# Optimization experiments

Measured on AMD Instinct MI355X. Metric: run time of the kernel, lower is better.

Reference implementation:

```python
import jax, jax.numpy as jnp
import numpy as np

B, T, H = 2, 2048, 1024
NH = 16
D = H // NH  # head_dim = 64
SCALE = D ** -0.5


def setup_inputs() -> dict:
    key = jax.random.key(0)
    ks = jax.random.split(key, 10)
    s_in = 1.0 / np.sqrt(H)   # torch Linear init scale for fan_in=H
    s_d = 1.0 / np.sqrt(D)
    return {
        "x":  jax.random.normal(ks[0], (B, T, H), jnp.float32),
        # stacked per-head Q/K projections: [NH, H, D] weights, [NH, D] biases
        "Wq": jax.random.uniform(ks[1], (NH, H, D), jnp.float32, -s_in, s_in),
        "bq": jax.random.uniform(ks[2], (NH, D), jnp.float32, -s_in, s_in),
        "Wk": jax.random.uniform(ks[3], (NH, H, D), jnp.float32, -s_in, s_in),
        "bk": jax.random.uniform(ks[4], (NH, D), jnp.float32, -s_in, s_in),
        # shared V projection H->D
        "Wv": jax.random.uniform(ks[5], (H, D), jnp.float32, -s_in, s_in),
        "bv": jax.random.uniform(ks[6], (D,), jnp.float32, -s_in, s_in),
        # out projection D->H
        "Wo": jax.random.uniform(ks[7], (D, H), jnp.float32, -s_d, s_d),
        "bo": jax.random.uniform(ks[8], (H,), jnp.float32, -s_d, s_d),
    }


def reference(x, Wq, bq, Wk, bk, Wv, bv, Wo, bo):
    # shared value projection: [B,T,D]
    v = jnp.einsum('bth,hd->btd', x, Wv) + bv
    # batched per-head Q/K projections: [NH,B,T,D]
    q = jnp.einsum('bth,nhd->nbtd', x, Wq) + bq[:, None, None, :]
    k = jnp.einsum('bth,nhd->nbtd', x, Wk) + bk[:, None, None, :]
    # scaled causal attention scores: [NH,B,T,T]
    scores = jnp.einsum('nbtd,nbsd->nbts', q, k) * SCALE
    causal = jnp.triu(jnp.ones((T, T), bool), k=1)  # True above diagonal
    scores = jnp.where(causal, -jnp.inf, scores)
    weights = jax.nn.softmax(scores, axis=-1)  # dropout is identity in eval
    # shared V attended per head, then mean over heads: [B,T,D]
    mean_head = jnp.einsum('nbts,bsd->btd', weights, v) / NH
    out = jnp.einsum('btd,dh->bth', mean_head, Wo) + bo
    mean_weights = jnp.mean(weights, axis=0)  # [B,T,T]
    return out, mean_weights
```

## Files before the change

### kernel.cpp

```cpp
#include <hip/hip_runtime.h>
#include <hip/hip_bf16.h>

#define B_ 2
#define T_ 2048
#define H_ 1024
#define NH_ 16
#define D_ 64
#define BT_ (B_*T_)
#define SCALE_ 0.125f

typedef _Float16 f16x8 __attribute__((ext_vector_type(8)));
typedef float f32x4 __attribute__((ext_vector_type(4)));

#define MFMA(a,b,c) __builtin_amdgcn_mfma_f32_16x16x32_f16((a),(b),(c),0,0,0)

typedef const __attribute__((address_space(1))) void GV;
typedef __attribute__((address_space(3))) void LV;

__device__ __forceinline__ size_t toff(int r, int c, int C) {
    return (size_t)((r >> 4) * (C >> 5) + (c >> 5)) * 512 + (size_t)(((c & 31) >> 3) * 128 + (r & 15) * 8 + (c & 7));
}
__device__ __forceinline__ f16x8 frag_ld(const _Float16* base, int rt, int kc, int Cc, int l15, int quad) {
    return *(const f16x8*)(base + (size_t)(rt * Cc + kc) * 512 + quad * 128 + l15 * 8);
}

__global__ __launch_bounds__(256) void k_cast_x(const float* __restrict__ x, _Float16* __restrict__ xb) {
    int idx = blockIdx.x * 256 + threadIdx.x;
    int t = idx >> 7, h0 = (idx & 127) * 8;
    const float* p = x + ((size_t)t << 10) + h0;
    float4 f0 = *(const float4*)p;
    float4 f1 = *(const float4*)(p + 4);
    f16x8 o;
    o[0]=(_Float16)f0.x; o[1]=(_Float16)f0.y; o[2]=(_Float16)f0.z; o[3]=(_Float16)f0.w;
    o[4]=(_Float16)f1.x; o[5]=(_Float16)f1.y; o[6]=(_Float16)f1.z; o[7]=(_Float16)f1.w;
    *(f16x8*)(xb + toff(t, h0, 1024)) = o;
}

__global__ __launch_bounds__(256) void k_cast_wqk(const float* __restrict__ Wq, const float* __restrict__ Wk,
                                                  _Float16* __restrict__ wqk) {
    int idx = blockIdx.x * 256 + threadIdx.x;
    int head = idx >> 13;
    int rem = idx & 8191;
    int h = rem >> 3;
    int d0 = (rem & 7) * 8;
    const float* pq = Wq + ((size_t)((head << 10) + h)) * 64 + d0;
    const float* pk = Wk + ((size_t)((head << 10) + h)) * 64 + d0;
    float4 q0 = *(const float4*)pq, q1 = *(const float4*)(pq + 4);
    float4 k0 = *(const float4*)pk, k1 = *(const float4*)(pk + 4);
    float qv[8] = {q0.x,q0.y,q0.z,q0.w,q1.x,q1.y,q1.z,q1.w};
    float kv[8] = {k0.x,k0.y,k0.z,k0.w,k1.x,k1.y,k1.z,k1.w};
#pragma unroll
    for (int e = 0; e < 8; e++) {
        int c = head * 64 + d0 + e;
        wqk[toff(c, h, 1024)]        = (_Float16)qv[e];
        wqk[toff(c + 1024, h, 1024)] = (_Float16)kv[e];
    }
}

__global__ __launch_bounds__(256) void k_cast_wvo(const float* __restrict__ Wv, const float* __restrict__ Wo,
                                                  _Float16* __restrict__ wvt, _Float16* __restrict__ wot) {
    int i = blockIdx.x * 256 + threadIdx.x;
    int d = i >> 10, h = i & 1023;
    wvt[toff(d, h, 1024)] = (_Float16)Wv[(size_t)h * 64 + d];
    int hh = i >> 6, dd = i & 63;
    wot[toff(hh, dd, 64)] = (_Float16)Wo[(size_t)dd * 1024 + hh];
}

__global__ __launch_bounds__(256) void k_gemm_qk(const _Float16* __restrict__ xb, const _Float16* __restrict__ wqk,
                                                 const float* __restrict__ bq, const float* __restrict__ bk,
                                                 _Float16* __restrict__ qh, _Float16* __restrict__ kh) {
    __shared__ __align__(16) _Float16 As[4096];
    __shared__ __align__(16) _Float16 Bs[4096];
    int bm = blockIdx.x >> 4, bn = blockIdx.x & 15;
    int tid = threadIdx.x, w = tid >> 6, lane = tid & 63, l15 = lane & 15, quad = lane >> 4;
    int rowbase = (w >> 1) * 64, colbase = (w & 1) * 64;
    f32x4 acc[4][4];
#pragma unroll
    for (int i = 0; i < 4; i++)
#pragma unroll
        for (int j = 0; j < 4; j++) acc[i][j] = (f32x4){0.f, 0.f, 0.f, 0.f};

    for (int kk = 0; kk < 32; kk++) {
        __syncthreads();
#pragma unroll
        for (int p = 0; p < 2; p++) {
            int c = w + p * 4;
            __builtin_amdgcn_global_load_lds((GV*)(xb  + ((size_t)((bm * 8 + c) * 32 + kk)) * 512 + lane * 8),
                                             (LV*)(As + c * 512 + lane * 8), 16, 0, 0);
            __builtin_amdgcn_global_load_lds((GV*)(wqk + ((size_t)((bn * 8 + c) * 32 + kk)) * 512 + lane * 8),
                                             (LV*)(Bs + c * 512 + lane * 8), 16, 0, 0);
        }
        __syncthreads();
        f16x8 a[4], bf[4];
#pragma unroll
        for (int i = 0; i < 4; i++) a[i]  = *(const f16x8*)&As[((rowbase >> 4) + i) * 512 + quad * 128 + l15 * 8];
#pragma unroll
        for (int j = 0; j < 4; j++) bf[j] = *(const f16x8*)&Bs[((colbase >> 4) + j) * 512 + quad * 128 + l15 * 8];
#pragma unroll
        for (int i = 0; i < 4; i++)
#pragma unroll
            for (int j = 0; j < 4; j++) acc[i][j] = MFMA(a[i], bf[j], acc[i][j]);
    }
    int b = (bm * 128) >> 11;
    int t_base = (bm * 128) & 2047;
    bool isq = (bn < 8);
    _Float16* dstbase = isq ? qh : kh;
#pragma unroll
    for (int j = 0; j < 4; j++) {
        int col = bn * 128 + colbase + j * 16 + l15;
        int c2 = isq ? col : col - 1024;
        int n = c2 >> 6, dd = c2 & 63;
        float bias = isq ? bq[c2] : bk[c2];
        _Float16* dst = dstbase + (size_t)(n * 2 + b) * 131072;
#pragma unroll
        for (int i = 0; i < 4; i++)
#pragma unroll
            for (int r = 0; r < 4; r++) {
                int t = t_base + rowbase + i * 16 + quad * 4 + r;
                float v = acc[i][j][r] + bias;
                if (isq) v *= SCALE_;
                dst[toff(t, dd, 64)] = (_Float16)v;
            }
    }
}

__global__ __launch_bounds__(256) void k_vproj(const _Float16* __restrict__ xb, const _Float16* __restrict__ wvt,
                                               const float* __restrict__ bv, _Float16* __restrict__ vt) {
    __shared__ float red[4][16][64];
    int tid = threadIdx.x, w = tid >> 6, lane = tid & 63, l15 = lane & 15, quad = lane >> 4;
    int rt = blockIdx.x;
    f32x4 acc[4];
#pragma unroll
    for (int j = 0; j < 4; j++) acc[j] = (f32x4){0.f, 0.f, 0.f, 0.f};
    for (int q = 0; q < 8; q++) {
        int kc = w * 8 + q;
        f16x8 a = frag_ld(xb, rt, kc, 32, l15, quad);
#pragma unroll
        for (int j = 0; j < 4; j++) {
            f16x8 bb = frag_ld(wvt, j, kc, 32, l15, quad);
            acc[j] = MFMA(a, bb, acc[j]);
        }
    }
#pragma unroll
    for (int j = 0; j < 4; j++)
#pragma unroll
        for (int r = 0; r < 4; r++) red[w][quad * 4 + r][j * 16 + l15] = acc[j][r];
    __syncthreads();
    int r = tid >> 4, dg = tid & 15;
    int b = rt >> 7, tt = (rt & 127) * 16 + r;
    _Float16* vtb = vt + (size_t)b * 131072;
#pragma unroll
    for (int e = 0; e < 4; e++) {
        int d = dg * 4 + e;
        float s = red[0][r][d] + red[1][r][d] + red[2][r][d] + red[3][r][d] + bv[d];
        vtb[toff(d, tt, 2048)] = (_Float16)s;
    }
}

__global__ __launch_bounds__(256) void k_pass1(const _Float16* __restrict__ qh, const _Float16* __restrict__ kh,
                                               float* __restrict__ lstat4) {
    int tid = threadIdx.x, w = tid >> 6, lane = tid & 63, l15 = lane & 15, quad = lane >> 4;
    int blk = blockIdx.x;
    int n = blk >> 6, b = (blk >> 5) & 1, strip = blk & 31;
    const _Float16* qb = qh + (size_t)(n * 2 + b) * 131072;
    const _Float16* kp = kh + (size_t)(n * 2 + b) * 131072;
    int rt0 = strip * 4;
    f16x8 aq[4][2];
#pragma unroll
    for (int i = 0; i < 4; i++)
#pragma unroll
        for (int kk = 0; kk < 2; kk++) aq[i][kk] = frag_ld(qb, rt0 + i, kk, 2, l15, quad);
    float l[4][4];
#pragma unroll
    for (int i = 0; i < 4; i++)
#pragma unroll
        for (int r = 0; r < 4; r++) l[i][r] = 0.f;
    int st_lo = w * (strip + 1);
    int st_hi = st_lo + strip + 1;
    for (int st = st_lo; st < st_hi; st++) {
        f16x8 k0 = frag_ld(kp, st, 0, 2, l15, quad);
        f16x8 k1 = frag_ld(kp, st, 1, 2, l15, quad);
#pragma unroll
        for (int i = 0; i < 4; i++) {
            if (st > rt0 + i) continue;
            f32x4 sc = (f32x4){0.f, 0.f, 0.f, 0.f};
            sc = MFMA(aq[i][0], k0, sc);
            sc = MFMA(aq[i][1], k1, sc);
            if (st == rt0 + i) {
#pragma unroll
                for (int r = 0; r < 4; r++)
                    if (l15 <= quad * 4 + r) l[i][r] += __expf(sc[r]);
            } else {
#pragma unroll
                for (int r = 0; r < 4; r++) l[i][r] += __expf(sc[r]);
            }
        }
    }
#pragma unroll
    for (int off = 1; off < 16; off <<= 1)
#pragma unroll
        for (int i = 0; i < 4; i++)
#pragma unroll
            for (int r = 0; r < 4; r++) l[i][r] += __shfl_xor(l[i][r], off, 64);
    if (l15 == 0) {
        int base = (n * 2 + b) * 2048 + strip * 64;
#pragma unroll
        for (int i = 0; i < 4; i++)
#pragma unroll
            for (int r = 0; r < 4; r++)
                lstat4[(size_t)(base + i * 16 + quad * 4 + r) * 4 + w] = l[i][r];
    }
}

__global__ __launch_bounds__(256) void k_zero(float* __restrict__ mw) {
    int bs = blockIdx.x;
    int s64 = bs & 31, q64 = (bs >> 5) & 31, b = bs >> 10;
    if (s64 <= q64) return;
    int tid = threadIdx.x;
    float4 z = {0.f, 0.f, 0.f, 0.f};
#pragma unroll
    for (int i = 0; i < 4; i++) {
        int idx = i * 256 + tid;
        int r = idx >> 4, c4 = idx & 15;
        *(float4*)&mw[(size_t)(b * T_ + q64 * 64 + r) * T_ + s64 * 64 + c4 * 4] = z;
    }
}

__global__ __launch_bounds__(256) void k_pass2(const _Float16* __restrict__ qh, const _Float16* __restrict__ kh,
                                               const float* __restrict__ lstat4,
                                               float* __restrict__ mw, _Float16* __restrict__ mwh) {
    int i0 = blockIdx.x;
    int b = (i0 >= 528) ? 1 : 0;
    int i = i0 - b * 528;
    int q64 = (int)((sqrtf(8.f * i + 1.f) - 1.f) * 0.5f);
    if ((q64 + 1) * (q64 + 2) / 2 <= i) q64++;
    else if (q64 * (q64 + 1) / 2 > i) q64--;
    int s64 = i - q64 * (q64 + 1) / 2;
    int tid = threadIdx.x;
    __shared__ float sl[16][64];
    for (int ii = tid; ii < 1024; ii += 256) {
        int h = ii >> 6, r = ii & 63;
        const float4 p = *(const float4*)&lstat4[(size_t)((h * 2 + b) * 2048 + q64 * 64 + r) * 4];
        sl[h][r] = 1.0f / (p.x + p.y + p.z + p.w);
    }
    __syncthreads();
    int w = tid >> 6, lane = tid & 63, l15 = lane & 15, quad = lane >> 4;
    int rw = (w >> 1) * 32, cw = (w & 1) * 32;
    int tg0 = q64 * 64 + rw, sg0 = s64 * 64 + cw;
    f32x4 macc[2][2];
#pragma unroll
    for (int ii = 0; ii < 2; ii++)
#pragma unroll
        for (int j = 0; j < 2; j++) macc[ii][j] = (f32x4){0.f, 0.f, 0.f, 0.f};

    for (int n = 0; n < NH_; n++) {
        const _Float16* qb = qh + (size_t)(n * 2 + b) * 131072;
        const _Float16* kp = kh + (size_t)(n * 2 + b) * 131072;
        f16x8 aq[2][2], kb[2][2];
#pragma unroll
        for (int ii = 0; ii < 2; ii++)
#pragma unroll
            for (int kk = 0; kk < 2; kk++) {
                aq[ii][kk] = frag_ld(qb, (tg0 >> 4) + ii, kk, 2, l15, quad);
                kb[ii][kk] = frag_ld(kp, (sg0 >> 4) + ii, kk, 2, l15, quad);
            }
#pragma unroll
        for (int ii = 0; ii < 2; ii++)
#pragma unroll
            for (int j = 0; j < 2; j++) {
                f32x4 sc = (f32x4){0.f, 0.f, 0.f, 0.f};
                sc = MFMA(aq[ii][0], kb[j][0], sc);
                sc = MFMA(aq[ii][1], kb[j][1], sc);
                int sg = sg0 + j * 16 + l15;
#pragma unroll
                for (int r = 0; r < 4; r++) {
                    int rloc = rw + ii * 16 + quad * 4 + r;
                    int tg = q64 * 64 + rloc;
                    float e = (sg <= tg) ? __expf(sc[r]) * sl[n][rloc] : 0.f;
                    macc[ii][j][r] += e;
                }
            }
    }
    float* mwb = mw + (size_t)b * T_ * T_;
    _Float16* mhb = mwh + (size_t)b * T_ * T_;
#pragma unroll
    for (int ii = 0; ii < 2; ii++)
#pragma unroll
        for (int j = 0; j < 2; j++)
#pragma unroll
            for (int r = 0; r < 4; r++) {
                int tg = q64 * 64 + rw + ii * 16 + quad * 4 + r;
                int sg = sg0 + j * 16 + l15;
                float v = macc[ii][j][r] * (1.f / 16.f);
                mwb[(size_t)tg * T_ + sg] = v;
                mhb[toff(tg, sg, 2048)] = (_Float16)v;
            }
}

__global__ __launch_bounds__(256) void k_pass3a(const _Float16* __restrict__ mwh, const _Float16* __restrict__ vt,
                                                _Float16* __restrict__ mhp) {
    __shared__ float red[4][16][64];
    int tid = threadIdx.x, w = tid >> 6, lane = tid & 63, l15 = lane & 15, quad = lane >> 4;
    int blk = blockIdx.x;
    int tile = blk >> 2, q = blk & 3;
    int b = tile >> 7, rtb = tile & 127;
    const _Float16* mb = mwh + (size_t)b * 4194304;
    const _Float16* vb = vt + (size_t)b * 131072;
    int nkc = (rtb * 16 + 47) >> 5;
    int qlo = q * 16;
    int qhi = min(qlo + 16, nkc);
    f32x4 acc[4];
#pragma unroll
    for (int j = 0; j < 4; j++) acc[j] = (f32x4){0.f, 0.f, 0.f, 0.f};
    for (int kc = qlo + w; kc < qhi; kc += 4) {
        f16x8 a = frag_ld(mb, rtb, kc, 64, l15, quad);
#pragma unroll
        for (int j = 0; j < 4; j++) {
            f16x8 bb = frag_ld(vb, j, kc, 64, l15, quad);
            acc[j] = MFMA(a, bb, acc[j]);
        }
    }
#pragma unroll
    for (int j = 0; j < 4; j++)
#pragma unroll
        for (int r = 0; r < 4; r++) red[w][quad * 4 + r][j * 16 + l15] = acc[j][r];
    __syncthreads();
    int r = tid >> 4, dg = tid & 15;
    _Float16* dst = mhp + (size_t)q * 262144;
#pragma unroll
    for (int e = 0; e < 4; e++) {
        int d = dg * 4 + e;
        float s = red[0][r][d] + red[1][r][d] + red[2][r][d] + red[3][r][d];
        dst[toff(tile * 16 + r, d, 64)] = (_Float16)s;
    }
}

__global__ __launch_bounds__(256) void k_pass3b(const _Float16* __restrict__ mhp, const _Float16* __restrict__ wot,
                                                const float* __restrict__ bo, float* __restrict__ out0) {
    int bm = blockIdx.x >> 4, bn = blockIdx.x & 15;
    int tid = threadIdx.x, w = tid >> 6, lane = tid & 63, l15 = lane & 15, quad = lane >> 4;
    int rt = bm * 4 + w;
    f16x8 a0[4], a1[4];
#pragma unroll
    for (int q = 0; q < 4; q++) {
        const _Float16* mb = mhp + (size_t)q * 262144;
        a0[q] = frag_ld(mb, rt, 0, 2, l15, quad);
        a1[q] = frag_ld(mb, rt, 1, 2, l15, quad);
    }
    f32x4 acc[4];
#pragma unroll
    for (int j = 0; j < 4; j++) acc[j] = (f32x4){0.f, 0.f, 0.f, 0.f};
#pragma unroll
    for (int j = 0; j < 4; j++) {
        f16x8 b0 = frag_ld(wot, bn * 4 + j, 0, 2, l15, quad);
        f16x8 b1 = frag_ld(wot, bn * 4 + j, 1, 2, l15, quad);
#pragma unroll
        for (int q = 0; q < 4; q++) {
            acc[j] = MFMA(a0[q], b0, acc[j]);
            acc[j] = MFMA(a1[q], b1, acc[j]);
        }
    }
#pragma unroll
    for (int j = 0; j < 4; j++)
#pragma unroll
        for (int r = 0; r < 4; r++) {
            int row = rt * 16 + quad * 4 + r;
            int col = bn * 64 + j * 16 + l15;
            out0[(size_t)row * 1024 + col] = acc[j][r] + bo[col];
        }
}

extern "C" void kernel_launch(void* const* d_in, const int* in_sizes, int n_in,
                              void* d_out, int out_size, void* d_ws, size_t ws_size,
                              hipStream_t stream) {
    const float* x  = (const float*)d_in[0];
    const float* Wq = (const float*)d_in[1];
    const float* bq = (const float*)d_in[2];
    const float* Wk = (const float*)d_in[3];
    const float* bk = (const float*)d_in[4];
    const float* Wv = (const float*)d_in[5];
    const float* bv = (const float*)d_in[6];
    const float* Wo = (const float*)d_in[7];
    const float* bo = (const float*)d_in[8];
    char* ws = (char*)d_ws;
    _Float16* xb    = (_Float16*)(ws + 0);
    _Float16* wqk   = (_Float16*)(ws + 8388608);
    _Float16* wvt   = (_Float16*)(ws + 12582912);
    _Float16* mwh   = (_Float16*)(ws + 0);
    _Float16* qh    = (_Float16*)(ws + 16777216);
    _Float16* kh    = (_Float16*)(ws + 25165824);
    _Float16* vt    = (_Float16*)(ws + 33554432);
    float*    lstat4= (float*)   (ws + 34078720);
    _Float16* mhp   = (_Float16*)(ws + 35127296);
    _Float16* wot   = (_Float16*)(ws + 37224448);
    float* out0 = (float*)d_out;
    float* mw   = out0 + (size_t)BT_ * H_;

    k_cast_x  <<<2048, 256, 0, stream>>>(x, xb);
    k_cast_wqk<<<512,  256, 0, stream>>>(Wq, Wk, wqk);
    k_cast_wvo<<<256,  256, 0, stream>>>(Wv, Wo, wvt, wot);
    k_zero    <<<2048, 256, 0, stream>>>(mw);
    k_gemm_qk <<<512,  256, 0, stream>>>(xb, wqk, bq, bk, qh, kh);
    k_vproj   <<<256,  256, 0, stream>>>(xb, wvt, bv, vt);
    k_pass1   <<<1024, 256, 0, stream>>>(qh, kh, lstat4);
    k_pass2   <<<1056, 256, 0, stream>>>(qh, kh, lstat4, mw, mwh);
    k_pass3a  <<<1024, 256, 0, stream>>>(mwh, vt, mhp);
    k_pass3b  <<<1024, 256, 0, stream>>>(mhp, wot, bo, out0);
}
```

Baseline: 217.5 us.

## Fuse prep kernels, split diagonal attention pass, use exp2 and prefetching

Merges the three cast kernels and the zero-fill of the upper triangle into one launch. The Q scale now folds in log2(e) so softmax can use hardware exp2. The weight-averaging pass is split into an unmasked off-diagonal kernel and a masked diagonal kernel, and the 1/16 head mean moves into the row normaliser. The QK GEMM epilogue stages tiles through LDS so global stores are vectorised, and the pass1, pass2 and pass3a loops get register double-buffered prefetch. The cost is extra register pressure and one more kernel launch for the diagonal blocks.

```diff
diff --git a/kernel.cpp b/kernel.cpp
--- a/kernel.cpp
+++ b/kernel.cpp
@@ -8,11 +8,13 @@
 #define D_ 64
 #define BT_ (B_*T_)
 #define SCALE_ 0.125f
+#define LOG2E_ 1.4426950408889634f
 
 typedef _Float16 f16x8 __attribute__((ext_vector_type(8)));
 typedef float f32x4 __attribute__((ext_vector_type(4)));
 
 #define MFMA(a,b,c) __builtin_amdgcn_mfma_f32_16x16x32_f16((a),(b),(c),0,0,0)
+#define EXP2(x) __builtin_amdgcn_exp2f(x)
 
 typedef const __attribute__((address_space(1))) void GV;
 typedef __attribute__((address_space(3))) void LV;
@@ -24,46 +26,63 @@
     return *(const f16x8*)(base + (size_t)(rt * Cc + kc) * 512 + quad * 128 + l15 * 8);
 }
 
-__global__ __launch_bounds__(256) void k_cast_x(const float* __restrict__ x, _Float16* __restrict__ xb) {
-    int idx = blockIdx.x * 256 + threadIdx.x;
-    int t = idx >> 7, h0 = (idx & 127) * 8;
-    const float* p = x + ((size_t)t << 10) + h0;
-    float4 f0 = *(const float4*)p;
-    float4 f1 = *(const float4*)(p + 4);
-    f16x8 o;
-    o[0]=(_Float16)f0.x; o[1]=(_Float16)f0.y; o[2]=(_Float16)f0.z; o[3]=(_Float16)f0.w;
-    o[4]=(_Float16)f1.x; o[5]=(_Float16)f1.y; o[6]=(_Float16)f1.z; o[7]=(_Float16)f1.w;
-    *(f16x8*)(xb + toff(t, h0, 1024)) = o;
-}
-
-__global__ __launch_bounds__(256) void k_cast_wqk(const float* __restrict__ Wq, const float* __restrict__ Wk,
-                                                  _Float16* __restrict__ wqk) {
-    int idx = blockIdx.x * 256 + threadIdx.x;
-    int head = idx >> 13;
-    int rem = idx & 8191;
-    int h = rem >> 3;
-    int d0 = (rem & 7) * 8;
-    const float* pq = Wq + ((size_t)((head << 10) + h)) * 64 + d0;
-    const float* pk = Wk + ((size_t)((head << 10) + h)) * 64 + d0;
-    float4 q0 = *(const float4*)pq, q1 = *(const float4*)(pq + 4);
-    float4 k0 = *(const float4*)pk, k1 = *(const float4*)(pk + 4);
-    float qv[8] = {q0.x,q0.y,q0.z,q0.w,q1.x,q1.y,q1.z,q1.w};
-    float kv[8] = {k0.x,k0.y,k0.z,k0.w,k1.x,k1.y,k1.z,k1.w};
-#pragma unroll
-    for (int e = 0; e < 8; e++) {
-        int c = head * 64 + d0 + e;
-        wqk[toff(c, h, 1024)]        = (_Float16)qv[e];
-        wqk[toff(c + 1024, h, 1024)] = (_Float16)kv[e];
-    }
-}
-
-__global__ __launch_bounds__(256) void k_cast_wvo(const float* __restrict__ Wv, const float* __restrict__ Wo,
-                                                  _Float16* __restrict__ wvt, _Float16* __restrict__ wot) {
-    int i = blockIdx.x * 256 + threadIdx.x;
-    int d = i >> 10, h = i & 1023;
-    wvt[toff(d, h, 1024)] = (_Float16)Wv[(size_t)h * 64 + d];
-    int hh = i >> 6, dd = i & 63;
-    wot[toff(hh, dd, 64)] = (_Float16)Wo[(size_t)dd * 1024 + hh];
+__global__ __launch_bounds__(256) void k_prep(const float* __restrict__ x,
+                                              const float* __restrict__ Wq, const float* __restrict__ Wk,
+                                              const float* __restrict__ Wv, const float* __restrict__ Wo,
+                                              _Float16* __restrict__ xb, _Float16* __restrict__ wqk,
+                                              _Float16* __restrict__ wvt, _Float16* __restrict__ wot,
+                                              float* __restrict__ mw) {
+    int blk = blockIdx.x, tid = threadIdx.x;
+    if (blk < 2048) {
+        int idx = blk * 256 + tid;
+        int t = idx >> 7, h0 = (idx & 127) * 8;
+        const float* p = x + ((size_t)t << 10) + h0;
+        float4 f0 = *(const float4*)p;
+        float4 f1 = *(const float4*)(p + 4);
+        f16x8 o;
+        o[0]=(_Float16)f0.x; o[1]=(_Float16)f0.y; o[2]=(_Float16)f0.z; o[3]=(_Float16)f0.w;
+        o[4]=(_Float16)f1.x; o[5]=(_Float16)f1.y; o[6]=(_Float16)f1.z; o[7]=(_Float16)f1.w;
+        *(f16x8*)(xb + toff(t, h0, 1024)) = o;
+    } else if (blk < 2560) {
+        int idx = (blk - 2048) * 256 + tid;
+        int head = idx >> 13;
+        int rem = idx & 8191;
+        int h = rem >> 3;
+        int d0 = (rem & 7) * 8;
+        const float* pq = Wq + ((size_t)((head << 10) + h)) * 64 + d0;
+        const float* pk = Wk + ((size_t)((head << 10) + h)) * 64 + d0;
+        float4 q0 = *(const float4*)pq, q1 = *(const float4*)(pq + 4);
+        float4 k0 = *(const float4*)pk, k1 = *(const float4*)(pk + 4);
+        float qv[8] = {q0.x,q0.y,q0.z,q0.w,q1.x,q1.y,q1.z,q1.w};
+        float kv[8] = {k0.x,k0.y,k0.z,k0.w,k1.x,k1.y,k1.z,k1.w};
+#pragma unroll
+        for (int e = 0; e < 8; e++) {
+            int c = head * 64 + d0 + e;
+            wqk[toff(c, h, 1024)]        = (_Float16)qv[e];
+            wqk[toff(c + 1024, h, 1024)] = (_Float16)kv[e];
+        }
+    } else if (blk < 2816) {
+        int i = (blk - 2560) * 256 + tid;
+        int d = i >> 10, h = i & 1023;
+        wvt[toff(d, h, 1024)] = (_Float16)Wv[(size_t)h * 64 + d];
+        int hh = i >> 6, dd = i & 63;
+        wot[toff(hh, dd, 64)] = (_Float16)Wo[(size_t)dd * 1024 + hh];
+    } else {
+        int iz = blk - 2816;
+        int b = (iz >= 496) ? 1 : 0;
+        int i = iz - b * 496;
+        int s64 = (int)((sqrtf(8.f * i + 1.f) + 1.f) * 0.5f);
+        if (s64 * (s64 - 1) / 2 > i) s64--;
+        if ((s64 + 1) * s64 / 2 <= i) s64++;
+        int q64 = i - s64 * (s64 - 1) / 2;
+        float4 z = {0.f, 0.f, 0.f, 0.f};
+#pragma unroll
+        for (int it = 0; it < 4; it++) {
+            int idx = it * 256 + tid;
+            int r = idx >> 4, c4 = idx & 15;
+            *(float4*)&mw[(size_t)(b * T_ + q64 * 64 + r) * T_ + s64 * 64 + c4 * 4] = z;
+        }
+    }
 }
 
 __global__ __launch_bounds__(256) void k_gemm_qk(const _Float16* __restrict__ xb, const _Float16* __restrict__ wqk,
@@ -101,26 +120,35 @@
 #pragma unroll
             for (int j = 0; j < 4; j++) acc[i][j] = MFMA(a[i], bf[j], acc[i][j]);
     }
+    __syncthreads();
     int b = (bm * 128) >> 11;
     int t_base = (bm * 128) & 2047;
+    int rtbase = (t_base + rowbase) >> 4;
     bool isq = (bn < 8);
-    _Float16* dstbase = isq ? qh : kh;
+    int c2base = isq ? (bn * 128 + colbase) : (bn * 128 + colbase - 1024);
+    int n = c2base >> 6;
+    _Float16* dst = (isq ? qh : kh) + (size_t)(n * 2 + b) * 131072;
+    const float* bias_p = isq ? bq : bk;
+    float qs = SCALE_ * LOG2E_;
+    int i2 = lane >> 4, rowrb = lane & 15;
 #pragma unroll
     for (int j = 0; j < 4; j++) {
-        int col = bn * 128 + colbase + j * 16 + l15;
-        int c2 = isq ? col : col - 1024;
-        int n = c2 >> 6, dd = c2 & 63;
-        float bias = isq ? bq[c2] : bk[c2];
-        _Float16* dst = dstbase + (size_t)(n * 2 + b) * 131072;
+        float bias = bias_p[c2base + j * 16 + l15];
+        _Float16* stg = ((j & 1) ? Bs : As) + w * 1024;
 #pragma unroll
         for (int i = 0; i < 4; i++)
 #pragma unroll
             for (int r = 0; r < 4; r++) {
-                int t = t_base + rowbase + i * 16 + quad * 4 + r;
                 float v = acc[i][j][r] + bias;
-                if (isq) v *= SCALE_;
-                dst[toff(t, dd, 64)] = (_Float16)v;
-            }
+                if (isq) v *= qs;
+                stg[(i * 16 + quad * 4 + r) * 16 + l15] = (_Float16)v;
+            }
+#pragma unroll
+        for (int oct = 0; oct < 2; oct++) {
+            f16x8 val = *(const f16x8*)&stg[(i2 * 16 + rowrb) * 16 + oct * 8];
+            int dd0 = j * 16 + oct * 8;
+            *(f16x8*)(dst + (size_t)((rtbase + i2) * 2 + (dd0 >> 5)) * 512 + ((dd0 & 31) >> 3) * 128 + rowrb * 8) = val;
+        }
     }
 }
 
@@ -177,24 +205,28 @@
         for (int r = 0; r < 4; r++) l[i][r] = 0.f;
     int st_lo = w * (strip + 1);
     int st_hi = st_lo + strip + 1;
+    f16x8 c0 = frag_ld(kp, st_lo, 0, 2, l15, quad);
+    f16x8 c1 = frag_ld(kp, st_lo, 1, 2, l15, quad);
     for (int st = st_lo; st < st_hi; st++) {
-        f16x8 k0 = frag_ld(kp, st, 0, 2, l15, quad);
-        f16x8 k1 = frag_ld(kp, st, 1, 2, l15, quad);
+        int sn = (st + 1 < st_hi) ? st + 1 : st;
+        f16x8 n0 = frag_ld(kp, sn, 0, 2, l15, quad);
+        f16x8 n1 = frag_ld(kp, sn, 1, 2, l15, quad);
 #pragma unroll
         for (int i = 0; i < 4; i++) {
             if (st > rt0 + i) continue;
             f32x4 sc = (f32x4){0.f, 0.f, 0.f, 0.f};
-            sc = MFMA(aq[i][0], k0, sc);
-            sc = MFMA(aq[i][1], k1, sc);
+            sc = MFMA(aq[i][0], c0, sc);
+            sc = MFMA(aq[i][1], c1, sc);
             if (st == rt0 + i) {
 #pragma unroll
                 for (int r = 0; r < 4; r++)
-                    if (l15 <= quad * 4 + r) l[i][r] += __expf(sc[r]);
+                    if (l15 <= quad * 4 + r) l[i][r] += EXP2(sc[r]);
             } else {
 #pragma unroll
-                for (int r = 0; r < 4; r++) l[i][r] += __expf(sc[r]);
-            }
-        }
+                for (int r = 0; r < 4; r++) l[i][r] += EXP2(sc[r]);
+            }
+        }
+        c0 = n0; c1 = n1;
     }
 #pragma unroll
     for (int off = 1; off < 16; off <<= 1)
@@ -212,47 +244,123 @@
     }
 }
 
-__global__ __launch_bounds__(256) void k_zero(float* __restrict__ mw) {
-    int bs = blockIdx.x;
-    int s64 = bs & 31, q64 = (bs >> 5) & 31, b = bs >> 10;
-    if (s64 <= q64) return;
+__global__ __launch_bounds__(256) void k_pass2o(const _Float16* __restrict__ qh, const _Float16* __restrict__ kh,
+                                                const float* __restrict__ lstat4,
+                                                float* __restrict__ mw, _Float16* __restrict__ mwh) {
+    int iz = blockIdx.x;
+    int b = (iz >= 496) ? 1 : 0;
+    int i = iz - b * 496;
+    int q64 = (int)((sqrtf(8.f * i + 1.f) + 1.f) * 0.5f);
+    if (q64 * (q64 - 1) / 2 > i) q64--;
+    if ((q64 + 1) * q64 / 2 <= i) q64++;
+    int s64 = i - q64 * (q64 - 1) / 2;
     int tid = threadIdx.x;
-    float4 z = {0.f, 0.f, 0.f, 0.f};
-#pragma unroll
-    for (int i = 0; i < 4; i++) {
-        int idx = i * 256 + tid;
-        int r = idx >> 4, c4 = idx & 15;
-        *(float4*)&mw[(size_t)(b * T_ + q64 * 64 + r) * T_ + s64 * 64 + c4 * 4] = z;
-    }
-}
-
-__global__ __launch_bounds__(256) void k_pass2(const _Float16* __restrict__ qh, const _Float16* __restrict__ kh,
-                                               const float* __restrict__ lstat4,
-                                               float* __restrict__ mw, _Float16* __restrict__ mwh) {
-    int i0 = blockIdx.x;
-    int b = (i0 >= 528) ? 1 : 0;
-    int i = i0 - b * 528;
-    int q64 = (int)((sqrtf(8.f * i + 1.f) - 1.f) * 0.5f);
-    if ((q64 + 1) * (q64 + 2) / 2 <= i) q64++;
-    else if (q64 * (q64 + 1) / 2 > i) q64--;
-    int s64 = i - q64 * (q64 + 1) / 2;
+    __shared__ float sl[16][64];
+    __shared__ __align__(16) _Float16 stg[4][1024];
+    for (int ii = tid; ii < 1024; ii += 256) {
+        int h = ii >> 6, r = ii & 63;
+        const float4 p = *(const float4*)&lstat4[(size_t)((h * 2 + b) * 2048 + q64 * 64 + r) * 4];
+        sl[h][r] = 0.0625f / (p.x + p.y + p.z + p.w);
+    }
+    __syncthreads();
+    int w = tid >> 6, lane = tid & 63, l15 = lane & 15, quad = lane >> 4;
+    int rw = (w >> 1) * 32, cw = (w & 1) * 32;
+    int rt0 = (q64 * 64 + rw) >> 4, st0 = (s64 * 64 + cw) >> 4;
+    f16x8 A[2][2][2], K[2][2][2];
+#pragma unroll
+    for (int ii = 0; ii < 2; ii++)
+#pragma unroll
+        for (int kk = 0; kk < 2; kk++) {
+            A[0][ii][kk] = frag_ld(qh + (size_t)b * 131072, rt0 + ii, kk, 2, l15, quad);
+            K[0][ii][kk] = frag_ld(kh + (size_t)b * 131072, st0 + ii, kk, 2, l15, quad);
+        }
+    f32x4 macc[2][2];
+#pragma unroll
+    for (int ii = 0; ii < 2; ii++)
+#pragma unroll
+        for (int j = 0; j < 2; j++) macc[ii][j] = (f32x4){0.f, 0.f, 0.f, 0.f};
+#pragma unroll
+    for (int n = 0; n < NH_; n++) {
+        int cur = n & 1;
+        if (n < NH_ - 1) {
+            const _Float16* qb = qh + (size_t)((n + 1) * 2 + b) * 131072;
+            const _Float16* kp = kh + (size_t)((n + 1) * 2 + b) * 131072;
+#pragma unroll
+            for (int ii = 0; ii < 2; ii++)
+#pragma unroll
+                for (int kk = 0; kk < 2; kk++) {
+                    A[cur ^ 1][ii][kk] = frag_ld(qb, rt0 + ii, kk, 2, l15, quad);
+                    K[cur ^ 1][ii][kk] = frag_ld(kp, st0 + ii, kk, 2, l15, quad);
+                }
+        }
+        f32x4 slv[2];
+#pragma unroll
+        for (int ii = 0; ii < 2; ii++) slv[ii] = *(const f32x4*)&sl[n][rw + ii * 16 + quad * 4];
+#pragma unroll
+        for (int ii = 0; ii < 2; ii++)
+#pragma unroll
+            for (int j = 0; j < 2; j++) {
+                f32x4 sc = (f32x4){0.f, 0.f, 0.f, 0.f};
+                sc = MFMA(A[cur][ii][0], K[cur][j][0], sc);
+                sc = MFMA(A[cur][ii][1], K[cur][j][1], sc);
+#pragma unroll
+                for (int r = 0; r < 4; r++) macc[ii][j][r] += EXP2(sc[r]) * slv[ii][r];
+            }
+    }
+    float* mwb = mw + (size_t)b * T_ * T_;
+#pragma unroll
+    for (int ii = 0; ii < 2; ii++)
+#pragma unroll
+        for (int j = 0; j < 2; j++)
+#pragma unroll
+            for (int r = 0; r < 4; r++) {
+                int tg = q64 * 64 + rw + ii * 16 + quad * 4 + r;
+                int sg = s64 * 64 + cw + j * 16 + l15;
+                mwb[(size_t)tg * T_ + sg] = macc[ii][j][r];
+            }
+    _Float16* ws16 = stg[w];
+#pragma unroll
+    for (int ii = 0; ii < 2; ii++)
+#pragma unroll
+        for (int j = 0; j < 2; j++)
+#pragma unroll
+            for (int r = 0; r < 4; r++) {
+                int cl = cw + j * 16 + l15;
+                int clw = j * 16 + l15;
+                (void)cl;
+                ws16[ii * 512 + (clw >> 3) * 128 + (quad * 4 + r) * 8 + (clw & 7)] = (_Float16)macc[ii][j][r];
+            }
+    _Float16* mhb = mwh + (size_t)b * 4194304;
+    int rowrb = lane & 15, qc = lane >> 4;
+#pragma unroll
+    for (int ii = 0; ii < 2; ii++) {
+        f16x8 val = *(const f16x8*)&ws16[ii * 512 + qc * 128 + rowrb * 8];
+        *(f16x8*)(mhb + (size_t)((rt0 + ii) * 64 + ((s64 * 64 + cw) >> 5)) * 512 + qc * 128 + rowrb * 8) = val;
+    }
+}
+
+__global__ __launch_bounds__(256) void k_pass2d(const _Float16* __restrict__ qh, const _Float16* __restrict__ kh,
+                                                const float* __restrict__ lstat4,
+                                                float* __restrict__ mw, _Float16* __restrict__ mwh) {
+    int blk = blockIdx.x;
+    int b = blk >> 5, q64 = blk & 31, s64 = q64;
     int tid = threadIdx.x;
     __shared__ float sl[16][64];
     for (int ii = tid; ii < 1024; ii += 256) {
         int h = ii >> 6, r = ii & 63;
         const float4 p = *(const float4*)&lstat4[(size_t)((h * 2 + b) * 2048 + q64 * 64 + r) * 4];
-        sl[h][r] = 1.0f / (p.x + p.y + p.z + p.w);
+        sl[h][r] = 0.0625f / (p.x + p.y + p.z + p.w);
     }
     __syncthreads();
     int w = tid >> 6, lane = tid & 63, l15 = lane & 15, quad = lane >> 4;
     int rw = (w >> 1) * 32, cw = (w & 1) * 32;
-    int tg0 = q64 * 64 + rw, sg0 = s64 * 64 + cw;
+    int rt0 = (q64 * 64 + rw) >> 4, st0 = (s64 * 64 + cw) >> 4;
     f32x4 macc[2][2];
 #pragma unroll
     for (int ii = 0; ii < 2; ii++)
 #pragma unroll
         for (int j = 0; j < 2; j++) macc[ii][j] = (f32x4){0.f, 0.f, 0.f, 0.f};
-
+#pragma unroll
     for (int n = 0; n < NH_; n++) {
         const _Float16* qb = qh + (size_t)(n * 2 + b) * 131072;
         const _Float16* kp = kh + (size_t)(n * 2 + b) * 131072;
@@ -261,9 +369,12 @@
         for (int ii = 0; ii < 2; ii++)
 #pragma unroll
             for (int kk = 0; kk < 2; kk++) {
-                aq[ii][kk] = frag_ld(qb, (tg0 >> 4) + ii, kk, 2, l15, quad);
-                kb[ii][kk] = frag_ld(kp, (sg0 >> 4) + ii, kk, 2, l15, quad);
-            }
+                aq[ii][kk] = frag_ld(qb, rt0 + ii, kk, 2, l15, quad);
+                kb[ii][kk] = frag_ld(kp, st0 + ii, kk, 2, l15, quad);
+            }
+        f32x4 slv[2];
+#pragma unroll
+        for (int ii = 0; ii < 2; ii++) slv[ii] = *(const f32x4*)&sl[n][rw + ii * 16 + quad * 4];
 #pragma unroll
         for (int ii = 0; ii < 2; ii++)
 #pragma unroll
@@ -271,18 +382,16 @@
                 f32x4 sc = (f32x4){0.f, 0.f, 0.f, 0.f};
                 sc = MFMA(aq[ii][0], kb[j][0], sc);
                 sc = MFMA(aq[ii][1], kb[j][1], sc);
-                int sg = sg0 + j * 16 + l15;
+                int sg = s64 * 64 + cw + j * 16 + l15;
 #pragma unroll
                 for (int r = 0; r < 4; r++) {
-                    int rloc = rw + ii * 16 + quad * 4 + r;
-                    int tg = q64 * 64 + rloc;
-                    float e = (sg <= tg) ? __expf(sc[r]) * sl[n][rloc] : 0.f;
-                    macc[ii][j][r] += e;
+                    int tg = q64 * 64 + rw + ii * 16 + quad * 4 + r;
+                    macc[ii][j][r] += (sg <= tg) ? EXP2(sc[r]) * slv[ii][r] : 0.f;
                 }
             }
     }
     float* mwb = mw + (size_t)b * T_ * T_;
-    _Float16* mhb = mwh + (size_t)b * T_ * T_;
+    _Float16* mhb = mwh + (size_t)b * 4194304;
 #pragma unroll
     for (int ii = 0; ii < 2; ii++)
 #pragma unroll
@@ -290,8 +399,8 @@
 #pragma unroll
             for (int r = 0; r < 4; r++) {
                 int tg = q64 * 64 + rw + ii * 16 + quad * 4 + r;
-                int sg = sg0 + j * 16 + l15;
-                float v = macc[ii][j][r] * (1.f / 16.f);
+                int sg = s64 * 64 + cw + j * 16 + l15;
+                float v = macc[ii][j][r];
                 mwb[(size_t)tg * T_ + sg] = v;
                 mhb[toff(tg, sg, 2048)] = (_Float16)v;
             }
@@ -312,12 +421,23 @@
     f32x4 acc[4];
 #pragma unroll
     for (int j = 0; j < 4; j++) acc[j] = (f32x4){0.f, 0.f, 0.f, 0.f};
-    for (int kc = qlo + w; kc < qhi; kc += 4) {
-        f16x8 a = frag_ld(mb, rtb, kc, 64, l15, quad);
-#pragma unroll
-        for (int j = 0; j < 4; j++) {
-            f16x8 bb = frag_ld(vb, j, kc, 64, l15, quad);
-            acc[j] = MFMA(a, bb, acc[j]);
+    int kc = qlo + w;
+    if (kc < qhi) {
+        f16x8 Ac = frag_ld(mb, rtb, kc, 64, l15, quad);
+        f16x8 Bc[4];
+#pragma unroll
+        for (int j = 0; j < 4; j++) Bc[j] = frag_ld(vb, j, kc, 64, l15, quad);
+        for (; kc < qhi; kc += 4) {
+            int kn = (kc + 4 < qhi) ? kc + 4 : kc;
+            f16x8 An = frag_ld(mb, rtb, kn, 64, l15, quad);
+            f16x8 Bn[4];
+#pragma unroll
+            for (int j = 0; j < 4; j++) Bn[j] = frag_ld(vb, j, kn, 64, l15, quad);
+#pragma unroll
+            for (int j = 0; j < 4; j++) acc[j] = MFMA(Ac, Bc[j], acc[j]);
+            Ac = An;
+#pragma unroll
+            for (int j = 0; j < 4; j++) Bc[j] = Bn[j];
         }
     }
 #pragma unroll
@@ -396,14 +516,12 @@
     float* out0 = (float*)d_out;
     float* mw   = out0 + (size_t)BT_ * H_;
 
-    k_cast_x  <<<2048, 256, 0, stream>>>(x, xb);
-    k_cast_wqk<<<512,  256, 0, stream>>>(Wq, Wk, wqk);
-    k_cast_wvo<<<256,  256, 0, stream>>>(Wv, Wo, wvt, wot);
-    k_zero    <<<2048, 256, 0, stream>>>(mw);
+    k_prep    <<<3808, 256, 0, stream>>>(x, Wq, Wk, Wv, Wo, xb, wqk, wvt, wot, mw);
     k_gemm_qk <<<512,  256, 0, stream>>>(xb, wqk, bq, bk, qh, kh);
     k_vproj   <<<256,  256, 0, stream>>>(xb, wvt, bv, vt);
     k_pass1   <<<1024, 256, 0, stream>>>(qh, kh, lstat4);
-    k_pass2   <<<1056, 256, 0, stream>>>(qh, kh, lstat4, mw, mwh);
+    k_pass2o  <<<992,  256, 0, stream>>>(qh, kh, lstat4, mw, mwh);
+    k_pass2d  <<<64,   256, 0, stream>>>(qh, kh, lstat4, mw, mwh);
     k_pass3a  <<<1024, 256, 0, stream>>>(mwh, vt, mhp);
     k_pass3b  <<<1024, 256, 0, stream>>>(mhp, wot, bo, out0);
 }
```

New measurement: 244.5 us. 1.12x slower.
